# Optimization experiments

Measured on AMD Instinct MI355X. Metric: run time of the kernel, lower is better.

The kernel has to match this reference:

```python
import jax, jax.numpy as jnp
import numpy as np

IO, H, S, N = 64, 1024, 512, 64

def setup_inputs() -> dict:
    key = jax.random.key(0)
    ks = jax.random.split(key, 6)
    scale = 0.05  # keep activations in a sane range for tanh/softmax
    return {
        "states": jax.random.normal(ks[0], (N, S, H), jnp.float32) * scale,
        "output_set": jax.random.normal(ks[1], (IO, H), jnp.float32) * scale,
        "Wo": jax.random.normal(ks[2], (2 * H, H), jnp.float32) * scale,
        "bo": jax.random.normal(ks[3], (H,), jnp.float32) * scale,
        "Wc": jax.random.normal(ks[4], (IO * H, IO), jnp.float32) * scale,
        "bc": jax.random.normal(ks[5], (IO,), jnp.float32) * scale,
    }

def reference(states, output_set, Wo, bo, Wc, bc):
    # Batched over the n_states Python loop of the original module.
    # attn scores: output_set [io,h] x states [n,s,h] -> [n,io,s]
    attn = jnp.einsum('ih,nsh->nis', output_set, states)
    attn = jax.nn.softmax(attn, axis=-1)  # softmax over context (sm_over_context=True)
    mix = jnp.einsum('nis,nsh->nih', attn, states)            # [n,io,h]
    out = jnp.broadcast_to(output_set[None], mix.shape)       # [n,io,h]
    combined = jnp.concatenate([mix, out], axis=-1)           # [n,io,2h]
    o = combined @ Wo + bo                                    # linear_out: 2h -> h
    logits = jnp.tanh(o).reshape(o.shape[0], -1) @ Wc + bc    # C: io*h -> io
    return logits
```

## Files before the change

### kernel.cpp

```cpp
#include <hip/hip_runtime.h>
#include <hip/hip_bf16.h>

#define IOdim 64
#define Hdim  1024
#define Sdim  512
#define Nbat  64

typedef __bf16 bf16x8_t __attribute__((ext_vector_type(8)));
typedef float  f32x4_t  __attribute__((ext_vector_type(4)));

#define MFMA16(a, b, c) __builtin_amdgcn_mfma_f32_16x16x32_bf16((a), (b), (c), 0, 0, 0)

__device__ __forceinline__ unsigned short f2bf(float f) {
    return __builtin_bit_cast(unsigned short, (__bf16)f);
}

__global__ __launch_bounds__(256) void cvt_kernel(const float* __restrict__ in,
                                                  unsigned short* __restrict__ outp,
                                                  int nElem) {
    int idx = blockIdx.x * 256 + threadIdx.x;
    if (idx < nElem) outp[idx] = f2bf(in[idx]);
}

__global__ __launch_bounds__(256) void transpose_cvt(const float* __restrict__ in,
                                                     unsigned short* __restrict__ outp,
                                                     int R, int C) {
    __shared__ float tile[32][33];
    int c0 = blockIdx.x * 32, r0 = blockIdx.y * 32;
    int tx = threadIdx.x, ty = threadIdx.y;
#pragma unroll
    for (int i = 0; i < 4; i++) {
        int r = ty + i * 8;
        tile[r][tx] = in[(size_t)(r0 + r) * C + c0 + tx];
    }
    __syncthreads();
#pragma unroll
    for (int i = 0; i < 4; i++) {
        int r = ty + i * 8;
        outp[(size_t)(c0 + r) * R + r0 + tx] = f2bf(tile[tx][r]);
    }
}

__global__ __launch_bounds__(256) void scores_kernel(const float* __restrict__ states,
                                                     const unsigned short* __restrict__ osb,
                                                     float* __restrict__ attnf) {
    __shared__ unsigned short Alds[64 * 40];
    int n = blockIdx.y;
    int tid = threadIdx.x, lane = tid & 63, g = tid >> 6;
    int col = lane & 15, quad = lane >> 4;
    int s = blockIdx.x * 64 + g * 16 + col;
    const float* srow = states + (n * Sdim + s) * Hdim + quad * 8;
    f32x4_t acc0 = {0,0,0,0}, acc1 = {0,0,0,0}, acc2 = {0,0,0,0}, acc3 = {0,0,0,0};
    for (int kc = 0; kc < Hdim; kc += 32) {
        uint4 av = *(const uint4*)(osb + lane * Hdim + kc + g * 8);
        *(uint4*)(Alds + lane * 40 + g * 8) = av;
        __syncthreads();
        float4 p0 = *(const float4*)(srow + kc);
        float4 p1 = *(const float4*)(srow + kc + 4);
        bf16x8_t b;
        b[0] = (__bf16)p0.x; b[1] = (__bf16)p0.y; b[2] = (__bf16)p0.z; b[3] = (__bf16)p0.w;
        b[4] = (__bf16)p1.x; b[5] = (__bf16)p1.y; b[6] = (__bf16)p1.z; b[7] = (__bf16)p1.w;
        bf16x8_t a0 = *(const bf16x8_t*)(Alds + (col)      * 40 + quad * 8);
        bf16x8_t a1 = *(const bf16x8_t*)(Alds + (16 + col) * 40 + quad * 8);
        bf16x8_t a2 = *(const bf16x8_t*)(Alds + (32 + col) * 40 + quad * 8);
        bf16x8_t a3 = *(const bf16x8_t*)(Alds + (48 + col) * 40 + quad * 8);
        acc0 = MFMA16(a0, b, acc0);
        acc1 = MFMA16(a1, b, acc1);
        acc2 = MFMA16(a2, b, acc2);
        acc3 = MFMA16(a3, b, acc3);
        __syncthreads();
    }
    f32x4_t accs[4] = {acc0, acc1, acc2, acc3};
    float* ob = attnf + (n * IOdim) * Sdim + blockIdx.x * 64 + g * 16 + col;
#pragma unroll
    for (int ai = 0; ai < 4; ai++)
#pragma unroll
        for (int r = 0; r < 4; r++) {
            int i = ai * 16 + quad * 4 + r;
            ob[i * Sdim] = accs[ai][r];
        }
}

__global__ __launch_bounds__(256) void softmax_kernel(const float* __restrict__ attnf,
                                                      unsigned short* __restrict__ attnb) {
    int row = blockIdx.x * 4 + (threadIdx.x >> 6);
    int lane = threadIdx.x & 63;
    const float* p = attnf + (size_t)row * Sdim + lane * 8;
    float4 v0 = ((const float4*)p)[0];
    float4 v1 = ((const float4*)p)[1];
    float v[8] = {v0.x, v0.y, v0.z, v0.w, v1.x, v1.y, v1.z, v1.w};
    float m = v[0];
#pragma unroll
    for (int j = 1; j < 8; j++) m = fmaxf(m, v[j]);
#pragma unroll
    for (int off = 32; off > 0; off >>= 1) m = fmaxf(m, __shfl_xor(m, off));
    float sum = 0.f;
#pragma unroll
    for (int j = 0; j < 8; j++) { v[j] = __expf(v[j] - m); sum += v[j]; }
#pragma unroll
    for (int off = 32; off > 0; off >>= 1) sum += __shfl_xor(sum, off);
    float inv = 1.0f / sum;
    union { unsigned short u[8]; uint4 q; } res;
#pragma unroll
    for (int j = 0; j < 8; j++) res.u[j] = f2bf(v[j] * inv);
    *(uint4*)(attnb + (size_t)row * Sdim + lane * 8) = res.q;
}

__global__ __launch_bounds__(256) void mix_kernel(const float* __restrict__ states,
                                                  const unsigned short* __restrict__ attnb,
                                                  unsigned short* __restrict__ mixb) {
    __shared__ unsigned short Tlds[64 * 40];
    __shared__ unsigned short Alds[64 * 40];
    int n = blockIdx.y, h0 = blockIdx.x * 64;
    int tid = threadIdx.x, lane = tid & 63, g = tid >> 6;
    int col = lane & 15, quad = lane >> 4;
    f32x4_t acc0 = {0,0,0,0}, acc1 = {0,0,0,0}, acc2 = {0,0,0,0}, acc3 = {0,0,0,0};
    for (int sc = 0; sc < Sdim; sc += 32) {
        union { unsigned short u[8]; uint4 q; } pk;
#pragma unroll
        for (int rep = 0; rep < 8; rep++) {
            int sl = g * 8 + rep;
            pk.u[rep] = f2bf(states[(n * Sdim + sc + sl) * Hdim + h0 + lane]);
        }
        *(uint4*)(Tlds + lane * 40 + g * 8) = pk.q;
        uint4 av = *(const uint4*)(attnb + (n * IOdim + lane) * Sdim + sc + g * 8);
        *(uint4*)(Alds + lane * 40 + g * 8) = av;
        __syncthreads();
        bf16x8_t b  = *(const bf16x8_t*)(Tlds + (g * 16 + col) * 40 + quad * 8);
        bf16x8_t a0 = *(const bf16x8_t*)(Alds + (col)      * 40 + quad * 8);
        bf16x8_t a1 = *(const bf16x8_t*)(Alds + (16 + col) * 40 + quad * 8);
        bf16x8_t a2 = *(const bf16x8_t*)(Alds + (32 + col) * 40 + quad * 8);
        bf16x8_t a3 = *(const bf16x8_t*)(Alds + (48 + col) * 40 + quad * 8);
        acc0 = MFMA16(a0, b, acc0);
        acc1 = MFMA16(a1, b, acc1);
        acc2 = MFMA16(a2, b, acc2);
        acc3 = MFMA16(a3, b, acc3);
        __syncthreads();
    }
    f32x4_t accs[4] = {acc0, acc1, acc2, acc3};
    int h = h0 + g * 16 + col;
#pragma unroll
    for (int ai = 0; ai < 4; ai++)
#pragma unroll
        for (int r = 0; r < 4; r++) {
            int i = ai * 16 + quad * 4 + r;
            mixb[(n * IOdim + i) * Hdim + h] = f2bf(accs[ai][r]);
        }
}

__global__ __launch_bounds__(256) void out_gemm(const unsigned short* __restrict__ mixb,
                                                const unsigned short* __restrict__ osb,
                                                const unsigned short* __restrict__ woT,
                                                const float* __restrict__ bo,
                                                unsigned short* __restrict__ tb) {
    __shared__ unsigned short Alds[64 * 40];
    int h0 = blockIdx.x * 64, r0 = blockIdx.y * 64;
    int tid = threadIdx.x, lane = tid & 63, g = tid >> 6;
    int col = lane & 15, quad = lane >> 4;
    f32x4_t acc0 = {0,0,0,0}, acc1 = {0,0,0,0}, acc2 = {0,0,0,0}, acc3 = {0,0,0,0};
    const unsigned short* brow = woT + (h0 + g * 16 + col) * 2048 + quad * 8;
    for (int kc = 0; kc < 2048; kc += 32) {
        int ks = kc + g * 8;
        uint4 av;
        if (ks < 1024) av = *(const uint4*)(mixb + (r0 + lane) * Hdim + ks);
        else           av = *(const uint4*)(osb + lane * Hdim + (ks - 1024));
        *(uint4*)(Alds + lane * 40 + g * 8) = av;
        __syncthreads();
        bf16x8_t b  = *(const bf16x8_t*)(brow + kc);
        bf16x8_t a0 = *(const bf16x8_t*)(Alds + (col)      * 40 + quad * 8);
        bf16x8_t a1 = *(const bf16x8_t*)(Alds + (16 + col) * 40 + quad * 8);
        bf16x8_t a2 = *(const bf16x8_t*)(Alds + (32 + col) * 40 + quad * 8);
        bf16x8_t a3 = *(const bf16x8_t*)(Alds + (48 + col) * 40 + quad * 8);
        acc0 = MFMA16(a0, b, acc0);
        acc1 = MFMA16(a1, b, acc1);
        acc2 = MFMA16(a2, b, acc2);
        acc3 = MFMA16(a3, b, acc3);
        __syncthreads();
    }
    f32x4_t accs[4] = {acc0, acc1, acc2, acc3};
    int h = h0 + g * 16 + col;
    float bov = bo[h];
#pragma unroll
    for (int ai = 0; ai < 4; ai++)
#pragma unroll
        for (int r = 0; r < 4; r++) {
            int rr = r0 + ai * 16 + quad * 4 + r;
            tb[rr * Hdim + h] = f2bf(tanhf(accs[ai][r] + bov));
        }
}

__global__ __launch_bounds__(256) void final_gemm(const unsigned short* __restrict__ tb,
                                                  const unsigned short* __restrict__ wcT,
                                                  float* __restrict__ partials) {
    __shared__ unsigned short Alds[64 * 40];
    int kc0 = blockIdx.x * 1024;
    int tid = threadIdx.x, lane = tid & 63, g = tid >> 6;
    int col = lane & 15, quad = lane >> 4;
    f32x4_t acc0 = {0,0,0,0}, acc1 = {0,0,0,0}, acc2 = {0,0,0,0}, acc3 = {0,0,0,0};
    const unsigned short* brow = wcT + (size_t)(g * 16 + col) * 65536 + quad * 8;
    for (int kc = kc0; kc < kc0 + 1024; kc += 32) {
        uint4 av = *(const uint4*)(tb + (size_t)lane * 65536 + kc + g * 8);
        *(uint4*)(Alds + lane * 40 + g * 8) = av;
        __syncthreads();
        bf16x8_t b  = *(const bf16x8_t*)(brow + kc);
        bf16x8_t a0 = *(const bf16x8_t*)(Alds + (col)      * 40 + quad * 8);
        bf16x8_t a1 = *(const bf16x8_t*)(Alds + (16 + col) * 40 + quad * 8);
        bf16x8_t a2 = *(const bf16x8_t*)(Alds + (32 + col) * 40 + quad * 8);
        bf16x8_t a3 = *(const bf16x8_t*)(Alds + (48 + col) * 40 + quad * 8);
        acc0 = MFMA16(a0, b, acc0);
        acc1 = MFMA16(a1, b, acc1);
        acc2 = MFMA16(a2, b, acc2);
        acc3 = MFMA16(a3, b, acc3);
        __syncthreads();
    }
    f32x4_t accs[4] = {acc0, acc1, acc2, acc3};
    int j = g * 16 + col;
    float* pb = partials + blockIdx.x * 4096;
#pragma unroll
    for (int ai = 0; ai < 4; ai++)
#pragma unroll
        for (int r = 0; r < 4; r++) {
            int nn = ai * 16 + quad * 4 + r;
            pb[nn * 64 + j] = accs[ai][r];
        }
}

__global__ __launch_bounds__(256) void reduce_kernel(const float* __restrict__ partials,
                                                     const float* __restrict__ bc,
                                                     float* __restrict__ out) {
    int idx = blockIdx.x * 256 + threadIdx.x;
    float s = bc[idx & 63];
#pragma unroll 8
    for (int b = 0; b < 64; b++) s += partials[b * 4096 + idx];
    out[idx] = s;
}

extern "C" void kernel_launch(void* const* d_in, const int* in_sizes, int n_in,
                              void* d_out, int out_size, void* d_ws, size_t ws_size,
                              hipStream_t stream) {
    const float* states     = (const float*)d_in[0];
    const float* output_set = (const float*)d_in[1];
    const float* Wo         = (const float*)d_in[2];
    const float* bo         = (const float*)d_in[3];
    const float* Wc         = (const float*)d_in[4];
    const float* bc         = (const float*)d_in[5];
    float* out = (float*)d_out;

    char* ws = (char*)d_ws;
    float*          attnf   = (float*)ws;
    unsigned short* attnb   = (unsigned short*)(ws + (8u  << 20));
    unsigned short* mixb    = (unsigned short*)(ws + (12u << 20));
    unsigned short* tb      = (unsigned short*)(ws + (20u << 20));
    unsigned short* woT     = (unsigned short*)(ws + (28u << 20));
    unsigned short* osb     = (unsigned short*)(ws + (32u << 20));
    unsigned short* wcT     = (unsigned short*)(ws + (32u << 20) + (1u << 18));
    float*          parts   = (float*)(ws + (41u << 20));

    cvt_kernel<<<dim3(IOdim * Hdim / 256), dim3(256), 0, stream>>>(output_set, osb, IOdim * Hdim);
    transpose_cvt<<<dim3(Hdim / 32, 2048 / 32), dim3(32, 8), 0, stream>>>(Wo, woT, 2048, Hdim);
    transpose_cvt<<<dim3(64 / 32, 65536 / 32), dim3(32, 8), 0, stream>>>(Wc, wcT, 65536, 64);
    scores_kernel<<<dim3(Sdim / 64, Nbat), dim3(256), 0, stream>>>(states, osb, attnf);
    softmax_kernel<<<dim3(Nbat * IOdim / 4), dim3(256), 0, stream>>>(attnf, attnb);
    mix_kernel<<<dim3(Hdim / 64, Nbat), dim3(256), 0, stream>>>(states, attnb, mixb);
    out_gemm<<<dim3(Hdim / 64, Nbat * IOdim / 64), dim3(256), 0, stream>>>(mixb, osb, woT, bo, tb);
    final_gemm<<<dim3(64), dim3(256), 0, stream>>>(tb, wcT, parts);
    reduce_kernel<<<dim3(16), dim3(256), 0, stream>>>(parts, bc, out);
}
```

Measured before the change: 356.4 us.

## Drop LDS staging for GEMM operands, widen out_gemm tile, split final_gemm K further

The scores, out_gemm and final_gemm kernels now read their bf16 A operands straight from global memory into MFMA registers instead of staging them through LDS with two barriers per K step. mix_kernel transposes 64 sequence rows per barrier pair instead of 32 and reads attention weights directly. out_gemm computes a 128-column tile per block, so each A fragment feeds eight MFMAs. final_gemm splits K across 256 blocks instead of 64 to fill more CUs, and the reduce kernel sums 256 partials. This trades fewer barriers and more parallelism for more redundant global/L2 traffic and a larger partial-sum buffer to reduce.

```diff
diff --git a/kernel.cpp b/kernel.cpp
--- a/kernel.cpp
+++ b/kernel.cpp
@@ -13,6 +13,12 @@
 
 __device__ __forceinline__ unsigned short f2bf(float f) {
     return __builtin_bit_cast(unsigned short, (__bf16)f);
+}
+__device__ __forceinline__ bf16x8_t cvt8(float4 p0, float4 p1) {
+    bf16x8_t b;
+    b[0] = (__bf16)p0.x; b[1] = (__bf16)p0.y; b[2] = (__bf16)p0.z; b[3] = (__bf16)p0.w;
+    b[4] = (__bf16)p1.x; b[5] = (__bf16)p1.y; b[6] = (__bf16)p1.z; b[7] = (__bf16)p1.w;
+    return b;
 }
 
 __global__ __launch_bounds__(256) void cvt_kernel(const float* __restrict__ in,
@@ -44,34 +50,28 @@
 __global__ __launch_bounds__(256) void scores_kernel(const float* __restrict__ states,
                                                      const unsigned short* __restrict__ osb,
                                                      float* __restrict__ attnf) {
-    __shared__ unsigned short Alds[64 * 40];
     int n = blockIdx.y;
     int tid = threadIdx.x, lane = tid & 63, g = tid >> 6;
     int col = lane & 15, quad = lane >> 4;
     int s = blockIdx.x * 64 + g * 16 + col;
-    const float* srow = states + (n * Sdim + s) * Hdim + quad * 8;
+    const float* srow = states + (size_t)(n * Sdim + s) * Hdim + quad * 8;
+    const unsigned short* ap = osb + (size_t)col * Hdim + quad * 8;
     f32x4_t acc0 = {0,0,0,0}, acc1 = {0,0,0,0}, acc2 = {0,0,0,0}, acc3 = {0,0,0,0};
     for (int kc = 0; kc < Hdim; kc += 32) {
-        uint4 av = *(const uint4*)(osb + lane * Hdim + kc + g * 8);
-        *(uint4*)(Alds + lane * 40 + g * 8) = av;
-        __syncthreads();
         float4 p0 = *(const float4*)(srow + kc);
         float4 p1 = *(const float4*)(srow + kc + 4);
-        bf16x8_t b;
-        b[0] = (__bf16)p0.x; b[1] = (__bf16)p0.y; b[2] = (__bf16)p0.z; b[3] = (__bf16)p0.w;
-        b[4] = (__bf16)p1.x; b[5] = (__bf16)p1.y; b[6] = (__bf16)p1.z; b[7] = (__bf16)p1.w;
-        bf16x8_t a0 = *(const bf16x8_t*)(Alds + (col)      * 40 + quad * 8);
-        bf16x8_t a1 = *(const bf16x8_t*)(Alds + (16 + col) * 40 + quad * 8);
-        bf16x8_t a2 = *(const bf16x8_t*)(Alds + (32 + col) * 40 + quad * 8);
-        bf16x8_t a3 = *(const bf16x8_t*)(Alds + (48 + col) * 40 + quad * 8);
+        bf16x8_t b  = cvt8(p0, p1);
+        bf16x8_t a0 = *(const bf16x8_t*)(ap + kc);
+        bf16x8_t a1 = *(const bf16x8_t*)(ap + 16 * Hdim + kc);
+        bf16x8_t a2 = *(const bf16x8_t*)(ap + 32 * Hdim + kc);
+        bf16x8_t a3 = *(const bf16x8_t*)(ap + 48 * Hdim + kc);
         acc0 = MFMA16(a0, b, acc0);
         acc1 = MFMA16(a1, b, acc1);
         acc2 = MFMA16(a2, b, acc2);
         acc3 = MFMA16(a3, b, acc3);
-        __syncthreads();
     }
     f32x4_t accs[4] = {acc0, acc1, acc2, acc3};
-    float* ob = attnf + (n * IOdim) * Sdim + blockIdx.x * 64 + g * 16 + col;
+    float* ob = attnf + (size_t)(n * IOdim) * Sdim + blockIdx.x * 64 + g * 16 + col;
 #pragma unroll
     for (int ai = 0; ai < 4; ai++)
 #pragma unroll
@@ -109,33 +109,33 @@
 __global__ __launch_bounds__(256) void mix_kernel(const float* __restrict__ states,
                                                   const unsigned short* __restrict__ attnb,
                                                   unsigned short* __restrict__ mixb) {
-    __shared__ unsigned short Tlds[64 * 40];
-    __shared__ unsigned short Alds[64 * 40];
+    __shared__ unsigned short Tlds[64 * 72];
     int n = blockIdx.y, h0 = blockIdx.x * 64;
     int tid = threadIdx.x, lane = tid & 63, g = tid >> 6;
     int col = lane & 15, quad = lane >> 4;
     f32x4_t acc0 = {0,0,0,0}, acc1 = {0,0,0,0}, acc2 = {0,0,0,0}, acc3 = {0,0,0,0};
-    for (int sc = 0; sc < Sdim; sc += 32) {
-        union { unsigned short u[8]; uint4 q; } pk;
-#pragma unroll
-        for (int rep = 0; rep < 8; rep++) {
-            int sl = g * 8 + rep;
-            pk.u[rep] = f2bf(states[(n * Sdim + sc + sl) * Hdim + h0 + lane]);
-        }
-        *(uint4*)(Tlds + lane * 40 + g * 8) = pk.q;
-        uint4 av = *(const uint4*)(attnb + (n * IOdim + lane) * Sdim + sc + g * 8);
-        *(uint4*)(Alds + lane * 40 + g * 8) = av;
+    const unsigned short* ap = attnb + (size_t)(n * IOdim + col) * Sdim + quad * 8;
+    for (int sc = 0; sc < Sdim; sc += 64) {
+        union { unsigned short u[16]; uint4 q[2]; } pk;
+        const float* sp = states + (size_t)(n * Sdim + sc + g * 16) * Hdim + h0 + lane;
+#pragma unroll
+        for (int rep = 0; rep < 16; rep++) pk.u[rep] = f2bf(sp[(size_t)rep * Hdim]);
+        if (sc) __syncthreads();
+        *(uint4*)(Tlds + lane * 72 + g * 16)     = pk.q[0];
+        *(uint4*)(Tlds + lane * 72 + g * 16 + 8) = pk.q[1];
         __syncthreads();
-        bf16x8_t b  = *(const bf16x8_t*)(Tlds + (g * 16 + col) * 40 + quad * 8);
-        bf16x8_t a0 = *(const bf16x8_t*)(Alds + (col)      * 40 + quad * 8);
-        bf16x8_t a1 = *(const bf16x8_t*)(Alds + (16 + col) * 40 + quad * 8);
-        bf16x8_t a2 = *(const bf16x8_t*)(Alds + (32 + col) * 40 + quad * 8);
-        bf16x8_t a3 = *(const bf16x8_t*)(Alds + (48 + col) * 40 + quad * 8);
-        acc0 = MFMA16(a0, b, acc0);
-        acc1 = MFMA16(a1, b, acc1);
-        acc2 = MFMA16(a2, b, acc2);
-        acc3 = MFMA16(a3, b, acc3);
-        __syncthreads();
+#pragma unroll
+        for (int ks = 0; ks < 64; ks += 32) {
+            bf16x8_t b  = *(const bf16x8_t*)(Tlds + (g * 16 + col) * 72 + ks + quad * 8);
+            bf16x8_t a0 = *(const bf16x8_t*)(ap + sc + ks);
+            bf16x8_t a1 = *(const bf16x8_t*)(ap + 16 * Sdim + sc + ks);
+            bf16x8_t a2 = *(const bf16x8_t*)(ap + 32 * Sdim + sc + ks);
+            bf16x8_t a3 = *(const bf16x8_t*)(ap + 48 * Sdim + sc + ks);
+            acc0 = MFMA16(a0, b, acc0);
+            acc1 = MFMA16(a1, b, acc1);
+            acc2 = MFMA16(a2, b, acc2);
+            acc3 = MFMA16(a3, b, acc3);
+        }
     }
     f32x4_t accs[4] = {acc0, acc1, acc2, acc3};
     int h = h0 + g * 16 + col;
@@ -144,7 +144,7 @@
 #pragma unroll
         for (int r = 0; r < 4; r++) {
             int i = ai * 16 + quad * 4 + r;
-            mixb[(n * IOdim + i) * Hdim + h] = f2bf(accs[ai][r]);
+            mixb[(size_t)(n * IOdim + i) * Hdim + h] = f2bf(accs[ai][r]);
         }
 }
 
@@ -153,65 +153,65 @@
                                                 const unsigned short* __restrict__ woT,
                                                 const float* __restrict__ bo,
                                                 unsigned short* __restrict__ tb) {
-    __shared__ unsigned short Alds[64 * 40];
-    int h0 = blockIdx.x * 64, r0 = blockIdx.y * 64;
+    int h0 = blockIdx.x * 128, r0 = blockIdx.y * 64;
+    int tid = threadIdx.x, lane = tid & 63, g = tid >> 6;
+    int col = lane & 15, quad = lane >> 4;
+    f32x4_t accA0 = {0,0,0,0}, accA1 = {0,0,0,0}, accA2 = {0,0,0,0}, accA3 = {0,0,0,0};
+    f32x4_t accB0 = {0,0,0,0}, accB1 = {0,0,0,0}, accB2 = {0,0,0,0}, accB3 = {0,0,0,0};
+    int h1 = h0 + g * 16 + col, h2 = h1 + 64;
+    const unsigned short* brow0 = woT + (size_t)h1 * 2048 + quad * 8;
+    const unsigned short* brow1 = woT + (size_t)h2 * 2048 + quad * 8;
+    const unsigned short* am = mixb + (size_t)(r0 + col) * Hdim + quad * 8;
+    const unsigned short* ao = osb + (size_t)col * Hdim + quad * 8;
+    for (int kc = 0; kc < 2048; kc += 32) {
+        const unsigned short* abase = (kc < 1024) ? (am + kc) : (ao + (kc - 1024));
+        bf16x8_t a0 = *(const bf16x8_t*)(abase);
+        bf16x8_t a1 = *(const bf16x8_t*)(abase + 16 * Hdim);
+        bf16x8_t a2 = *(const bf16x8_t*)(abase + 32 * Hdim);
+        bf16x8_t a3 = *(const bf16x8_t*)(abase + 48 * Hdim);
+        bf16x8_t b0 = *(const bf16x8_t*)(brow0 + kc);
+        bf16x8_t b1 = *(const bf16x8_t*)(brow1 + kc);
+        accA0 = MFMA16(a0, b0, accA0);
+        accA1 = MFMA16(a1, b0, accA1);
+        accA2 = MFMA16(a2, b0, accA2);
+        accA3 = MFMA16(a3, b0, accA3);
+        accB0 = MFMA16(a0, b1, accB0);
+        accB1 = MFMA16(a1, b1, accB1);
+        accB2 = MFMA16(a2, b1, accB2);
+        accB3 = MFMA16(a3, b1, accB3);
+    }
+    f32x4_t accsA[4] = {accA0, accA1, accA2, accA3};
+    f32x4_t accsB[4] = {accB0, accB1, accB2, accB3};
+    float bo1 = bo[h1], bo2 = bo[h2];
+#pragma unroll
+    for (int ai = 0; ai < 4; ai++)
+#pragma unroll
+        for (int r = 0; r < 4; r++) {
+            int rr = r0 + ai * 16 + quad * 4 + r;
+            tb[(size_t)rr * Hdim + h1] = f2bf(tanhf(accsA[ai][r] + bo1));
+            tb[(size_t)rr * Hdim + h2] = f2bf(tanhf(accsB[ai][r] + bo2));
+        }
+}
+
+__global__ __launch_bounds__(256) void final_gemm(const unsigned short* __restrict__ tb,
+                                                  const unsigned short* __restrict__ wcT,
+                                                  float* __restrict__ partials) {
+    int kc0 = blockIdx.x * 256;
     int tid = threadIdx.x, lane = tid & 63, g = tid >> 6;
     int col = lane & 15, quad = lane >> 4;
     f32x4_t acc0 = {0,0,0,0}, acc1 = {0,0,0,0}, acc2 = {0,0,0,0}, acc3 = {0,0,0,0};
-    const unsigned short* brow = woT + (h0 + g * 16 + col) * 2048 + quad * 8;
-    for (int kc = 0; kc < 2048; kc += 32) {
-        int ks = kc + g * 8;
-        uint4 av;
-        if (ks < 1024) av = *(const uint4*)(mixb + (r0 + lane) * Hdim + ks);
-        else           av = *(const uint4*)(osb + lane * Hdim + (ks - 1024));
-        *(uint4*)(Alds + lane * 40 + g * 8) = av;
-        __syncthreads();
-        bf16x8_t b  = *(const bf16x8_t*)(brow + kc);
-        bf16x8_t a0 = *(const bf16x8_t*)(Alds + (col)      * 40 + quad * 8);
-        bf16x8_t a1 = *(const bf16x8_t*)(Alds + (16 + col) * 40 + quad * 8);
-        bf16x8_t a2 = *(const bf16x8_t*)(Alds + (32 + col) * 40 + quad * 8);
-        bf16x8_t a3 = *(const bf16x8_t*)(Alds + (48 + col) * 40 + quad * 8);
+    const unsigned short* ap = tb + (size_t)col * 65536 + kc0 + quad * 8;
+    const unsigned short* bp = wcT + (size_t)(g * 16 + col) * 65536 + kc0 + quad * 8;
+    for (int kc = 0; kc < 256; kc += 32) {
+        bf16x8_t b  = *(const bf16x8_t*)(bp + kc);
+        bf16x8_t a0 = *(const bf16x8_t*)(ap + kc);
+        bf16x8_t a1 = *(const bf16x8_t*)(ap + (size_t)16 * 65536 + kc);
+        bf16x8_t a2 = *(const bf16x8_t*)(ap + (size_t)32 * 65536 + kc);
+        bf16x8_t a3 = *(const bf16x8_t*)(ap + (size_t)48 * 65536 + kc);
         acc0 = MFMA16(a0, b, acc0);
         acc1 = MFMA16(a1, b, acc1);
         acc2 = MFMA16(a2, b, acc2);
         acc3 = MFMA16(a3, b, acc3);
-        __syncthreads();
-    }
-    f32x4_t accs[4] = {acc0, acc1, acc2, acc3};
-    int h = h0 + g * 16 + col;
-    float bov = bo[h];
-#pragma unroll
-    for (int ai = 0; ai < 4; ai++)
-#pragma unroll
-        for (int r = 0; r < 4; r++) {
-            int rr = r0 + ai * 16 + quad * 4 + r;
-            tb[rr * Hdim + h] = f2bf(tanhf(accs[ai][r] + bov));
-        }
-}
-
-__global__ __launch_bounds__(256) void final_gemm(const unsigned short* __restrict__ tb,
-                                                  const unsigned short* __restrict__ wcT,
-                                                  float* __restrict__ partials) {
-    __shared__ unsigned short Alds[64 * 40];
-    int kc0 = blockIdx.x * 1024;
-    int tid = threadIdx.x, lane = tid & 63, g = tid >> 6;
-    int col = lane & 15, quad = lane >> 4;
-    f32x4_t acc0 = {0,0,0,0}, acc1 = {0,0,0,0}, acc2 = {0,0,0,0}, acc3 = {0,0,0,0};
-    const unsigned short* brow = wcT + (size_t)(g * 16 + col) * 65536 + quad * 8;
-    for (int kc = kc0; kc < kc0 + 1024; kc += 32) {
-        uint4 av = *(const uint4*)(tb + (size_t)lane * 65536 + kc + g * 8);
-        *(uint4*)(Alds + lane * 40 + g * 8) = av;
-        __syncthreads();
-        bf16x8_t b  = *(const bf16x8_t*)(brow + kc);
-        bf16x8_t a0 = *(const bf16x8_t*)(Alds + (col)      * 40 + quad * 8);
-        bf16x8_t a1 = *(const bf16x8_t*)(Alds + (16 + col) * 40 + quad * 8);
-        bf16x8_t a2 = *(const bf16x8_t*)(Alds + (32 + col) * 40 + quad * 8);
-        bf16x8_t a3 = *(const bf16x8_t*)(Alds + (48 + col) * 40 + quad * 8);
-        acc0 = MFMA16(a0, b, acc0);
-        acc1 = MFMA16(a1, b, acc1);
-        acc2 = MFMA16(a2, b, acc2);
-        acc3 = MFMA16(a3, b, acc3);
-        __syncthreads();
     }
     f32x4_t accs[4] = {acc0, acc1, acc2, acc3};
     int j = g * 16 + col;
@@ -231,7 +231,7 @@
     int idx = blockIdx.x * 256 + threadIdx.x;
     float s = bc[idx & 63];
 #pragma unroll 8
-    for (int b = 0; b < 64; b++) s += partials[b * 4096 + idx];
+    for (int b = 0; b < 256; b++) s += partials[b * 4096 + idx];
     out[idx] = s;
 }
 
@@ -247,14 +247,14 @@
     float* out = (float*)d_out;
 
     char* ws = (char*)d_ws;
-    float*          attnf   = (float*)ws;
-    unsigned short* attnb   = (unsigned short*)(ws + (8u  << 20));
-    unsigned short* mixb    = (unsigned short*)(ws + (12u << 20));
-    unsigned short* tb      = (unsigned short*)(ws + (20u << 20));
-    unsigned short* woT     = (unsigned short*)(ws + (28u << 20));
-    unsigned short* osb     = (unsigned short*)(ws + (32u << 20));
-    unsigned short* wcT     = (unsigned short*)(ws + (32u << 20) + (1u << 18));
-    float*          parts   = (float*)(ws + (41u << 20));
+    float*          attnf = (float*)ws;
+    unsigned short* attnb = (unsigned short*)(ws + (8u  << 20));
+    unsigned short* mixb  = (unsigned short*)(ws + (12u << 20));
+    unsigned short* tb    = (unsigned short*)(ws + (20u << 20));
+    unsigned short* woT   = (unsigned short*)(ws + (28u << 20));
+    unsigned short* osb   = (unsigned short*)(ws + (32u << 20));
+    unsigned short* wcT   = (unsigned short*)(ws + (32u << 20) + (1u << 18));
+    float*          parts = (float*)(ws + (41u << 20));
 
     cvt_kernel<<<dim3(IOdim * Hdim / 256), dim3(256), 0, stream>>>(output_set, osb, IOdim * Hdim);
     transpose_cvt<<<dim3(Hdim / 32, 2048 / 32), dim3(32, 8), 0, stream>>>(Wo, woT, 2048, Hdim);
@@ -262,7 +262,7 @@
     scores_kernel<<<dim3(Sdim / 64, Nbat), dim3(256), 0, stream>>>(states, osb, attnf);
     softmax_kernel<<<dim3(Nbat * IOdim / 4), dim3(256), 0, stream>>>(attnf, attnb);
     mix_kernel<<<dim3(Hdim / 64, Nbat), dim3(256), 0, stream>>>(states, attnb, mixb);
-    out_gemm<<<dim3(Hdim / 64, Nbat * IOdim / 64), dim3(256), 0, stream>>>(mixb, osb, woT, bo, tb);
-    final_gemm<<<dim3(64), dim3(256), 0, stream>>>(tb, wcT, parts);
+    out_gemm<<<dim3(Hdim / 128, Nbat * IOdim / 64), dim3(256), 0, stream>>>(mixb, osb, woT, bo, tb);
+    final_gemm<<<dim3(256), dim3(256), 0, stream>>>(tb, wcT, parts);
     reduce_kernel<<<dim3(16), dim3(256), 0, stream>>>(parts, bc, out);
 }
```

After: 381.6 us. 7.1% more time.
